# Performance work log

Hardware: AMD Instinct MI355X
Metric: run time of the kernel (lower is better)

## Reference

```python
import jax, jax.numpy as jnp
import numpy as np

NUM_EXPERTS = 4
TOPK = 1
TEMPERATURE = 1.0
NORM_TOPK_PROB = True
N_CLS = 1
N_REL = 4


def setup_inputs() -> dict:
    key = jax.random.key(0)
    ks = jax.random.split(key, 7)
    B, N_total, D, r, E = 64, 1029, 768, 64, NUM_EXPERTS
    x = jax.random.normal(ks[0], (B, N_total, D), dtype=jnp.float32)
    # parameters (torch Linear convention: weight [out, in])
    Wd = jax.random.normal(ks[1], (r, D), dtype=jnp.float32) * (1.0 / np.sqrt(D))
    Wg = jax.random.normal(ks[2], (E, r), dtype=jnp.float32) * (1.0 / np.sqrt(r))
    We = jax.random.normal(ks[3], (E, r, r), dtype=jnp.float32) * (1.0 / np.sqrt(r))
    be = jax.random.normal(ks[4], (E, r), dtype=jnp.float32) * 0.01
    Wu = jax.random.normal(ks[5], (D, r), dtype=jnp.float32) * (1.0 / np.sqrt(r))
    gamma = jnp.ones((D,), dtype=jnp.float32)  # LayerScale init_values=1.0
    return {"x": x, "Wd": Wd, "Wg": Wg, "We": We, "be": be, "Wu": Wu, "gamma": gamma}


def reference(x, Wd, Wg, We, be, Wu, gamma):
    # proj_down (bias=False) + exact GELU (nn.GELU default)
    h = jax.nn.gelu(jnp.einsum('bnd,rd->bnr', x, Wd), approximate=False)  # [B,Nt,r]
    cls_tok = h[:, :N_CLS, :]
    rel_tok = h[:, N_CLS:N_CLS + N_REL, :]
    t = h[:, N_CLS + N_REL:, :]                                           # [B,N,r]
    B, N, r = t.shape

    # gating: softmax scores, top-k selection
    logits = jnp.einsum('bnr,er->bne', t, Wg) / TEMPERATURE
    scores = jax.nn.softmax(logits, axis=-1)                              # [B,N,E]
    topk_w, topk_idx = jax.lax.top_k(scores, TOPK)                        # [B,N,K]
    if TOPK > 1 and NORM_TOPK_PROB:
        topk_w = topk_w / jnp.sum(topk_w, axis=-1, keepdims=True)

    # experts are tiny Linear(r,r): compute all experts densely, then gather.
    # Same math as per-expert gather/GEMM/scatter-combine in the source.
    expert_all = jnp.einsum('bnr,esr->bnes', t, We) + be                  # [B,N,E,r]
    idx_b = jnp.broadcast_to(topk_idx[..., None], (B, N, TOPK, r))
    sel = jnp.take_along_axis(expert_all, idx_b, axis=2)                  # [B,N,K,r]
    combine = jnp.sum(sel * topk_w[..., None], axis=2)                    # [B,N,r]

    full = jnp.concatenate([cls_tok, rel_tok, t + combine], axis=1)       # [B,Nt,r]
    # proj_up (bias=False) + LayerScale
    return jnp.einsum('bnr,dr->bnd', full, Wu) * gamma
```

## Files before the change

### kernel.cpp

```cpp
#include <hip/hip_runtime.h>
#include <math.h>


#define GELU(v) (0.5f*(v)*(1.0f + erff((v)*0.70710678118654752440f)))

typedef __attribute__((ext_vector_type(8))) short bf16x8;
typedef __attribute__((ext_vector_type(4))) float f32x4;

#define MFMA(a,b,c) __builtin_amdgcn_mfma_f32_16x16x32_bf16((a),(b),(c),0,0,0)

__device__ __forceinline__ unsigned pk_hi(float a, float b) {
  return (__float_as_uint(a) >> 16) | (__float_as_uint(b) & 0xFFFF0000u);
}
__device__ __forceinline__ float f_lo(float a) {
  return a - __uint_as_float(__float_as_uint(a) & 0xFFFF0000u);
}
union U8 { unsigned u[4]; bf16x8 v; uint4 q; };
__device__ __forceinline__ bf16x8 hi8(float4 f0, float4 f1) {
  U8 r; r.u[0]=pk_hi(f0.x,f0.y); r.u[1]=pk_hi(f0.z,f0.w);
        r.u[2]=pk_hi(f1.x,f1.y); r.u[3]=pk_hi(f1.z,f1.w); return r.v;
}
__device__ __forceinline__ bf16x8 lo8(float4 f0, float4 f1) {
  U8 r; r.u[0]=pk_hi(f_lo(f0.x),f_lo(f0.y)); r.u[1]=pk_hi(f_lo(f0.z),f_lo(f0.w));
        r.u[2]=pk_hi(f_lo(f1.x),f_lo(f1.y)); r.u[3]=pk_hi(f_lo(f1.z),f_lo(f1.w)); return r.v;
}

__device__ __forceinline__ void cp16(const char* g, char* d, int lane) {
#if __has_builtin(__builtin_amdgcn_global_load_lds)
  __builtin_amdgcn_global_load_lds(
      (const __attribute__((address_space(1))) unsigned int*)g,
      (__attribute__((address_space(3))) unsigned int*)d, 16, 0, 0);
#else
  *(uint4*)(d + lane*16) = *(const uint4*)g;
#endif
}

__global__ __launch_bounds__(256) void prep_pack(
    const float* __restrict__ Wd, const float* __restrict__ Wg,
    const float* __restrict__ We, const float* __restrict__ Wu,
    char* __restrict__ wp)
{
  int fid = blockIdx.x*4 + (threadIdx.x >> 6);
  if (fid >= 456) return;
  int l = threadIdx.x & 63, lg = l >> 4, lr = l & 15;
  float v[8];
  int part = 0;
  if (fid < 192) {
    int c = fid >> 3, s = fid & 7;
    int kt = c >> 1, kc = c & 1, nt = s >> 1; part = s & 1;
    const float* p = Wd + (size_t)(nt*16 + lr)*768 + kt*64 + kc*32 + lg*8;
    #pragma unroll
    for (int e = 0; e < 8; ++e) v[e] = p[e];
  } else if (fid < 264) {
    int f = fid - 192, ch = f >> 3, s = f & 7;
    if (ch == 0) {
      part = s & 1;
      int kc = (s >> 1) & 1;
      if (s < 4 && lr < 4) {
        const float* p = Wg + lr*64 + kc*32 + lg*8;
        #pragma unroll
        for (int e = 0; e < 8; ++e) v[e] = p[e];
      } else {
        #pragma unroll
        for (int e = 0; e < 8; ++e) v[e] = 0.f;
      }
    } else {
      int e_ = (ch - 1) >> 1, kc = (ch - 1) & 1, j = s >> 1; part = s & 1;
      const float* p = We + (size_t)(e_*64 + j*16 + lr)*64 + kc*32 + lg*8;
      #pragma unroll
      for (int e = 0; e < 8; ++e) v[e] = p[e];
    }
  } else {
    int f = fid - 264;
    int nt = f >> 2, kc = (f >> 1) & 1; part = f & 1;
    const float* p = Wu + (size_t)(nt*16 + lr)*64 + kc*32 + lg*8;
    #pragma unroll
    for (int e = 0; e < 8; ++e) v[e] = p[e];
  }
  U8 rr;
  if (part == 0) {
    rr.u[0]=pk_hi(v[0],v[1]); rr.u[1]=pk_hi(v[2],v[3]);
    rr.u[2]=pk_hi(v[4],v[5]); rr.u[3]=pk_hi(v[6],v[7]);
  } else {
    rr.u[0]=pk_hi(f_lo(v[0]),f_lo(v[1])); rr.u[1]=pk_hi(f_lo(v[2]),f_lo(v[3]));
    rr.u[2]=pk_hi(f_lo(v[4]),f_lo(v[5])); rr.u[3]=pk_hi(f_lo(v[6]),f_lo(v[7]));
  }
  *(uint4*)(wp + (size_t)fid*1024 + (size_t)l*16) = rr.q;
}

__global__ __launch_bounds__(256, 4) void fused(
    const float* __restrict__ x, const float* __restrict__ be,
    const float* __restrict__ gamma, const char* __restrict__ wp,
    float* __restrict__ out)
{
  __shared__ float sF[4][16][68];
  __shared__ char stage[2][8192];
  const int tid = threadIdx.x, bm = blockIdx.x;
  const int wv = tid >> 6, l = tid & 63, lg = l >> 4, lr = l & 15;
  const int tokbase = bm*64 + wv*16 + lg*4;

#define STAGE(chunk, buf) do { \
    const char* _g = wp + (size_t)(chunk)*8192 + (size_t)(wv*2)*1024 + (size_t)l*16; \
    char* _d = &stage[buf][wv*2048]; \
    cp16(_g, _d, l); \
    cp16(_g + 1024, _d + 1024, l); \
  } while (0)

  const float* xrow = x + (size_t)(bm*64 + wv*16 + lr)*768 + lg*8;
  f32x4 t4[4];
  #pragma unroll
  for (int nt = 0; nt < 4; ++nt)
    #pragma unroll
    for (int r = 0; r < 4; ++r) t4[nt][r] = 0.f;

  float4 xa = *(const float4*)xrow, xb = *(const float4*)(xrow + 4);
  STAGE(0, 0);
  __syncthreads();
  for (int c = 0; c < 24; ++c) {
    float4 xa2 = xa, xb2 = xb;
    if (c < 23) {
      STAGE(c + 1, (c + 1) & 1);
      const float* xp = xrow + (c + 1)*32;
      xa2 = *(const float4*)xp; xb2 = *(const float4*)(xp + 4);
    }
    bf16x8 ah = hi8(xa, xb), al = lo8(xa, xb);
    const char* bp = &stage[c & 1][l*16];
    #pragma unroll
    for (int nt = 0; nt < 4; ++nt) {
      bf16x8 bh = *(const bf16x8*)(bp + (size_t)(nt*2)*1024);
      bf16x8 bl = *(const bf16x8*)(bp + (size_t)(nt*2 + 1)*1024);
      t4[nt] = MFMA(ah, bh, t4[nt]);
      t4[nt] = MFMA(ah, bl, t4[nt]);
      t4[nt] = MFMA(al, bh, t4[nt]);
    }
    __syncthreads();
    xa = xa2; xb = xb2;
  }

  STAGE(24, 0);
  STAGE(25, 1);
  #pragma unroll
  for (int nt = 0; nt < 4; ++nt)
    #pragma unroll
    for (int r = 0; r < 4; ++r) {
      float g = GELU(t4[nt][r]);
      t4[nt][r] = g;
      sF[wv][lg*4 + r][nt*16 + lr] = g;
    }
  bf16x8 pah[2], pal[2];
  #pragma unroll
  for (int kc = 0; kc < 2; ++kc) {
    const float* ap = &sF[wv][lr][kc*32 + lg*8];
    float4 a0 = *(const float4*)ap, a1 = *(const float4*)(ap + 4);
    pah[kc] = hi8(a0, a1); pal[kc] = lo8(a0, a1);
  }
  __syncthreads();

  f32x4 lac;
  #pragma unroll
  for (int r = 0; r < 4; ++r) lac[r] = 0.f;
  {
    const char* bp = &stage[0][l*16];
    bf16x8 b0h = *(const bf16x8*)(bp);
    bf16x8 b0l = *(const bf16x8*)(bp + 1024);
    bf16x8 b1h = *(const bf16x8*)(bp + 2048);
    bf16x8 b1l = *(const bf16x8*)(bp + 3072);
    lac = MFMA(pah[0], b0h, lac); lac = MFMA(pah[0], b0l, lac); lac = MFMA(pal[0], b0h, lac);
    lac = MFMA(pah[1], b1h, lac); lac = MFMA(pah[1], b1l, lac); lac = MFMA(pal[1], b1h, lac);
  }
  float w_[4]; int ei_[4];
  #pragma unroll
  for (int r = 0; r < 4; ++r) {
    float lt = lac[r];
    int base = l & 48;
    float l0 = __shfl(lt, base + 0), l1 = __shfl(lt, base + 1);
    float l2 = __shfl(lt, base + 2), l3 = __shfl(lt, base + 3);
    int ei = 0; float lm = l0;
    if (l1 > lm) { lm = l1; ei = 1; }
    if (l2 > lm) { lm = l2; ei = 2; }
    if (l3 > lm) { lm = l3; ei = 3; }
    float s = expf(l0 - lm) + expf(l1 - lm) + expf(l2 - lm) + expf(l3 - lm);
    float w = 1.0f / s;
    int pos = (tokbase + r) % 1029;
    if (pos < 5) w = 0.0f;
    w_[r] = w; ei_[r] = ei;
  }
  __syncthreads();
  STAGE(26, 0);

  f32x4 de[4], sel[4];
  #pragma unroll
  for (int j = 0; j < 4; ++j)
    #pragma unroll
    for (int r = 0; r < 4; ++r) { de[j][r] = 0.f; sel[j][r] = 0.f; }

  #pragma unroll
  for (int s = 1; s <= 8; ++s) {
    const int e_ = (s - 1) >> 1, kc = (s - 1) & 1, cb = s & 1;
    const char* bp = &stage[cb][l*16];
    #pragma unroll
    for (int j = 0; j < 4; ++j) {
      bf16x8 bh = *(const bf16x8*)(bp + (size_t)(j*2)*1024);
      bf16x8 bl = *(const bf16x8*)(bp + (size_t)(j*2 + 1)*1024);
      de[j] = MFMA(pah[kc], bh, de[j]);
      de[j] = MFMA(pah[kc], bl, de[j]);
      de[j] = MFMA(pal[kc], bh, de[j]);
    }
    if (kc == 1) {
      #pragma unroll
      for (int j = 0; j < 4; ++j)
        #pragma unroll
        for (int r = 0; r < 4; ++r) {
          sel[j][r] = (ei_[r] == e_) ? de[j][r] : sel[j][r];
          de[j][r] = 0.f;
        }
    }
    __syncthreads();
    if (s <= 6) STAGE(26 + s, cb);
  }

  STAGE(33, 1);
  STAGE(34, 0);
  #pragma unroll
  for (int r = 0; r < 4; ++r)
    #pragma unroll
    for (int j = 0; j < 4; ++j) {
      int col = j*16 + lr;
      float full = t4[j][r] + w_[r] * (sel[j][r] + be[ei_[r]*64 + col]);
      sF[wv][lg*4 + r][col] = full;
    }
  bf16x8 a3h[2], a3l[2];
  #pragma unroll
  for (int kc = 0; kc < 2; ++kc) {
    const float* ap = &sF[wv][lr][kc*32 + lg*8];
    float4 a0 = *(const float4*)ap, a1 = *(const float4*)(ap + 4);
    a3h[kc] = hi8(a0, a1); a3l[kc] = lo8(a0, a1);
  }
  __syncthreads();

  for (int c = 0; c < 24; ++c) {
    const int cb = (c + 1) & 1;
    const char* bpc = &stage[cb][l*16];
    #pragma unroll
    for (int u = 0; u < 2; ++u) {
      const char* bp = bpc + u*4096;
      bf16x8 b0h = *(const bf16x8*)(bp);
      bf16x8 b0l = *(const bf16x8*)(bp + 1024);
      bf16x8 b1h = *(const bf16x8*)(bp + 2048);
      bf16x8 b1l = *(const bf16x8*)(bp + 3072);
      f32x4 o;
      #pragma unroll
      for (int r = 0; r < 4; ++r) o[r] = 0.f;
      o = MFMA(a3h[0], b0h, o); o = MFMA(a3h[0], b0l, o); o = MFMA(a3l[0], b0h, o);
      o = MFMA(a3h[1], b1h, o); o = MFMA(a3h[1], b1l, o); o = MFMA(a3l[1], b1h, o);
      const int col = (c*2 + u)*16 + lr;
      const float gv = gamma[col];
      #pragma unroll
      for (int r = 0; r < 4; ++r)
        out[(size_t)(tokbase + r)*768 + col] = o[r] * gv;
    }
    __syncthreads();
    if (c + 2 < 24) STAGE(35 + c, cb);
  }
#undef STAGE
}

extern "C" void kernel_launch(void* const* d_in, const int* in_sizes, int n_in,
                              void* d_out, int out_size, void* d_ws, size_t ws_size,
                              hipStream_t stream) {
  const float* x     = (const float*)d_in[0];
  const float* Wd    = (const float*)d_in[1];
  const float* Wg    = (const float*)d_in[2];
  const float* We    = (const float*)d_in[3];
  const float* be    = (const float*)d_in[4];
  const float* Wu    = (const float*)d_in[5];
  const float* gamma = (const float*)d_in[6];
  float* out = (float*)d_out;
  char* wp   = (char*)d_ws;

  prep_pack<<<114, 256, 0, stream>>>(Wd, Wg, We, Wu, wp);
  fused<<<1029, 256, 0, stream>>>(x, be, gamma, (const char*)wp, out);
}
```

Baseline: 428.7 us.

## Load packed weights directly into registers and drop LDS staging and barriers

Removes the double-buffered LDS stage and its global_load_lds copies. Each wave now reads the pre-packed bf16 weight fragments straight from global memory (L2-resident) into register double buffers, which eliminates almost all __syncthreads. It also adds a 4-deep register prefetch queue for x, preloads the expert biases to replace a gathered load, and lowers the occupancy hint to 3 waves because register pressure grows. The trade-off is redundant per-wave global/L2 traffic for the weights and lower occupancy.

```diff
diff --git a/kernel.cpp b/kernel.cpp
--- a/kernel.cpp
+++ b/kernel.cpp
@@ -23,16 +23,6 @@
 __device__ __forceinline__ bf16x8 lo8(float4 f0, float4 f1) {
   U8 r; r.u[0]=pk_hi(f_lo(f0.x),f_lo(f0.y)); r.u[1]=pk_hi(f_lo(f0.z),f_lo(f0.w));
         r.u[2]=pk_hi(f_lo(f1.x),f_lo(f1.y)); r.u[3]=pk_hi(f_lo(f1.z),f_lo(f1.w)); return r.v;
-}
-
-__device__ __forceinline__ void cp16(const char* g, char* d, int lane) {
-#if __has_builtin(__builtin_amdgcn_global_load_lds)
-  __builtin_amdgcn_global_load_lds(
-      (const __attribute__((address_space(1))) unsigned int*)g,
-      (__attribute__((address_space(3))) unsigned int*)d, 16, 0, 0);
-#else
-  *(uint4*)(d + lane*16) = *(const uint4*)g;
-#endif
 }
 
 __global__ __launch_bounds__(256) void prep_pack(
@@ -88,23 +78,16 @@
   *(uint4*)(wp + (size_t)fid*1024 + (size_t)l*16) = rr.q;
 }
 
-__global__ __launch_bounds__(256, 4) void fused(
+__global__ __launch_bounds__(256, 3) void fused(
     const float* __restrict__ x, const float* __restrict__ be,
     const float* __restrict__ gamma, const char* __restrict__ wp,
     float* __restrict__ out)
 {
   __shared__ float sF[4][16][68];
-  __shared__ char stage[2][8192];
   const int tid = threadIdx.x, bm = blockIdx.x;
   const int wv = tid >> 6, l = tid & 63, lg = l >> 4, lr = l & 15;
   const int tokbase = bm*64 + wv*16 + lg*4;
-
-#define STAGE(chunk, buf) do { \
-    const char* _g = wp + (size_t)(chunk)*8192 + (size_t)(wv*2)*1024 + (size_t)l*16; \
-    char* _d = &stage[buf][wv*2048]; \
-    cp16(_g, _d, l); \
-    cp16(_g + 1024, _d + 1024, l); \
-  } while (0)
+  const char* wpL = wp + (size_t)l*16;
 
   const float* xrow = x + (size_t)(bm*64 + wv*16 + lr)*768 + lg*8;
   f32x4 t4[4];
@@ -113,32 +96,66 @@
     #pragma unroll
     for (int r = 0; r < 4; ++r) t4[nt][r] = 0.f;
 
-  float4 xa = *(const float4*)xrow, xb = *(const float4*)(xrow + 4);
-  STAGE(0, 0);
-  __syncthreads();
-  for (int c = 0; c < 24; ++c) {
-    float4 xa2 = xa, xb2 = xb;
-    if (c < 23) {
-      STAGE(c + 1, (c + 1) & 1);
-      const float* xp = xrow + (c + 1)*32;
-      xa2 = *(const float4*)xp; xb2 = *(const float4*)(xp + 4);
-    }
-    bf16x8 ah = hi8(xa, xb), al = lo8(xa, xb);
-    const char* bp = &stage[c & 1][l*16];
-    #pragma unroll
-    for (int nt = 0; nt < 4; ++nt) {
-      bf16x8 bh = *(const bf16x8*)(bp + (size_t)(nt*2)*1024);
-      bf16x8 bl = *(const bf16x8*)(bp + (size_t)(nt*2 + 1)*1024);
-      t4[nt] = MFMA(ah, bh, t4[nt]);
-      t4[nt] = MFMA(ah, bl, t4[nt]);
-      t4[nt] = MFMA(al, bh, t4[nt]);
-    }
-    __syncthreads();
-    xa = xa2; xb = xb2;
-  }
-
-  STAGE(24, 0);
-  STAGE(25, 1);
+  float4 xqa[4], xqb[4];
+  #pragma unroll
+  for (int i = 0; i < 4; ++i) {
+    xqa[i] = *(const float4*)(xrow + i*32);
+    xqb[i] = *(const float4*)(xrow + i*32 + 4);
+  }
+  bf16x8 Bb[2][8];
+  #pragma unroll
+  for (int s = 0; s < 8; ++s)
+    Bb[0][s] = *(const bf16x8*)(wpL + (size_t)s*1024);
+
+#define P1_STEP(CBASE, I, DO_REFILL, DO_PF) do {                              \
+    const int c_ = (CBASE) + (I);                                             \
+    if (DO_PF) {                                                              \
+      _Pragma("unroll")                                                       \
+      for (int s = 0; s < 8; ++s)                                             \
+        Bb[((I)+1)&1][s] =                                                    \
+            *(const bf16x8*)(wpL + (size_t)((c_+1)*8 + s)*1024);              \
+    }                                                                         \
+    bf16x8 ah = hi8(xqa[(I)&3], xqb[(I)&3]);                                  \
+    bf16x8 al = lo8(xqa[(I)&3], xqb[(I)&3]);                                  \
+    if (DO_REFILL) {                                                          \
+      xqa[(I)&3] = *(const float4*)(xrow + (c_+4)*32);                        \
+      xqb[(I)&3] = *(const float4*)(xrow + (c_+4)*32 + 4);                    \
+    }                                                                         \
+    _Pragma("unroll")                                                         \
+    for (int nt = 0; nt < 4; ++nt) {                                          \
+      t4[nt] = MFMA(ah, Bb[(I)&1][nt*2],   t4[nt]);                           \
+      t4[nt] = MFMA(ah, Bb[(I)&1][nt*2+1], t4[nt]);                           \
+      t4[nt] = MFMA(al, Bb[(I)&1][nt*2],   t4[nt]);                           \
+    }                                                                         \
+  } while (0)
+
+  for (int cc = 0; cc < 20; cc += 4) {
+    P1_STEP(cc, 0, 1, 1);
+    P1_STEP(cc, 1, 1, 1);
+    P1_STEP(cc, 2, 1, 1);
+    P1_STEP(cc, 3, 1, 1);
+  }
+  P1_STEP(20, 0, 0, 1);
+  P1_STEP(20, 1, 0, 1);
+  P1_STEP(20, 2, 0, 1);
+  P1_STEP(20, 3, 0, 0);
+#undef P1_STEP
+
+  float beq[4][4];
+  #pragma unroll
+  for (int e = 0; e < 4; ++e)
+    #pragma unroll
+    for (int j = 0; j < 4; ++j)
+      beq[e][j] = be[e*64 + j*16 + lr];
+  bf16x8 g0h = *(const bf16x8*)(wpL + (size_t)192*1024);
+  bf16x8 g0l = *(const bf16x8*)(wpL + (size_t)193*1024);
+  bf16x8 g1h = *(const bf16x8*)(wpL + (size_t)194*1024);
+  bf16x8 g1l = *(const bf16x8*)(wpL + (size_t)195*1024);
+  bf16x8 Eb[2][8];
+  #pragma unroll
+  for (int s = 0; s < 8; ++s)
+    Eb[0][s] = *(const bf16x8*)(wpL + (size_t)(200 + s)*1024);
+
   #pragma unroll
   for (int nt = 0; nt < 4; ++nt)
     #pragma unroll
@@ -154,20 +171,13 @@
     float4 a0 = *(const float4*)ap, a1 = *(const float4*)(ap + 4);
     pah[kc] = hi8(a0, a1); pal[kc] = lo8(a0, a1);
   }
-  __syncthreads();
 
   f32x4 lac;
   #pragma unroll
   for (int r = 0; r < 4; ++r) lac[r] = 0.f;
-  {
-    const char* bp = &stage[0][l*16];
-    bf16x8 b0h = *(const bf16x8*)(bp);
-    bf16x8 b0l = *(const bf16x8*)(bp + 1024);
-    bf16x8 b1h = *(const bf16x8*)(bp + 2048);
-    bf16x8 b1l = *(const bf16x8*)(bp + 3072);
-    lac = MFMA(pah[0], b0h, lac); lac = MFMA(pah[0], b0l, lac); lac = MFMA(pal[0], b0h, lac);
-    lac = MFMA(pah[1], b1h, lac); lac = MFMA(pah[1], b1l, lac); lac = MFMA(pal[1], b1h, lac);
-  }
+  lac = MFMA(pah[0], g0h, lac); lac = MFMA(pah[0], g0l, lac); lac = MFMA(pal[0], g0h, lac);
+  lac = MFMA(pah[1], g1h, lac); lac = MFMA(pah[1], g1l, lac); lac = MFMA(pal[1], g1h, lac);
+
   float w_[4]; int ei_[4];
   #pragma unroll
   for (int r = 0; r < 4; ++r) {
@@ -185,8 +195,6 @@
     if (pos < 5) w = 0.0f;
     w_[r] = w; ei_[r] = ei;
   }
-  __syncthreads();
-  STAGE(26, 0);
 
   f32x4 de[4], sel[4];
   #pragma unroll
@@ -195,18 +203,21 @@
     for (int r = 0; r < 4; ++r) { de[j][r] = 0.f; sel[j][r] = 0.f; }
 
   #pragma unroll
-  for (int s = 1; s <= 8; ++s) {
-    const int e_ = (s - 1) >> 1, kc = (s - 1) & 1, cb = s & 1;
-    const char* bp = &stage[cb][l*16];
+  for (int st = 0; st < 8; ++st) {
+    if (st < 7) {
+      #pragma unroll
+      for (int s = 0; s < 8; ++s)
+        Eb[(st+1)&1][s] = *(const bf16x8*)(wpL + (size_t)(200 + (st+1)*8 + s)*1024);
+    }
+    const int kc = st & 1;
     #pragma unroll
     for (int j = 0; j < 4; ++j) {
-      bf16x8 bh = *(const bf16x8*)(bp + (size_t)(j*2)*1024);
-      bf16x8 bl = *(const bf16x8*)(bp + (size_t)(j*2 + 1)*1024);
-      de[j] = MFMA(pah[kc], bh, de[j]);
-      de[j] = MFMA(pah[kc], bl, de[j]);
-      de[j] = MFMA(pal[kc], bh, de[j]);
+      de[j] = MFMA(pah[kc], Eb[st&1][j*2],   de[j]);
+      de[j] = MFMA(pah[kc], Eb[st&1][j*2+1], de[j]);
+      de[j] = MFMA(pal[kc], Eb[st&1][j*2],   de[j]);
     }
     if (kc == 1) {
+      const int e_ = st >> 1;
       #pragma unroll
       for (int j = 0; j < 4; ++j)
         #pragma unroll
@@ -215,19 +226,19 @@
           de[j][r] = 0.f;
         }
     }
-    __syncthreads();
-    if (s <= 6) STAGE(26 + s, cb);
-  }
-
-  STAGE(33, 1);
-  STAGE(34, 0);
+  }
+
   #pragma unroll
   for (int r = 0; r < 4; ++r)
     #pragma unroll
     for (int j = 0; j < 4; ++j) {
-      int col = j*16 + lr;
-      float full = t4[j][r] + w_[r] * (sel[j][r] + be[ei_[r]*64 + col]);
-      sF[wv][lg*4 + r][col] = full;
+      float b0 = beq[0][j], b1 = beq[1][j], b2 = beq[2][j], b3 = beq[3][j];
+      float bsel = b0;
+      bsel = (ei_[r] == 1) ? b1 : bsel;
+      bsel = (ei_[r] == 2) ? b2 : bsel;
+      bsel = (ei_[r] == 3) ? b3 : bsel;
+      float full = t4[j][r] + w_[r] * (sel[j][r] + bsel);
+      sF[wv][lg*4 + r][j*16 + lr] = full;
     }
   bf16x8 a3h[2], a3l[2];
   #pragma unroll
@@ -236,33 +247,43 @@
     float4 a0 = *(const float4*)ap, a1 = *(const float4*)(ap + 4);
     a3h[kc] = hi8(a0, a1); a3l[kc] = lo8(a0, a1);
   }
-  __syncthreads();
-
-  for (int c = 0; c < 24; ++c) {
-    const int cb = (c + 1) & 1;
-    const char* bpc = &stage[cb][l*16];
-    #pragma unroll
-    for (int u = 0; u < 2; ++u) {
-      const char* bp = bpc + u*4096;
-      bf16x8 b0h = *(const bf16x8*)(bp);
-      bf16x8 b0l = *(const bf16x8*)(bp + 1024);
-      bf16x8 b1h = *(const bf16x8*)(bp + 2048);
-      bf16x8 b1l = *(const bf16x8*)(bp + 3072);
-      f32x4 o;
-      #pragma unroll
-      for (int r = 0; r < 4; ++r) o[r] = 0.f;
-      o = MFMA(a3h[0], b0h, o); o = MFMA(a3h[0], b0l, o); o = MFMA(a3l[0], b0h, o);
-      o = MFMA(a3h[1], b1h, o); o = MFMA(a3h[1], b1l, o); o = MFMA(a3l[1], b1h, o);
-      const int col = (c*2 + u)*16 + lr;
-      const float gv = gamma[col];
-      #pragma unroll
-      for (int r = 0; r < 4; ++r)
-        out[(size_t)(tokbase + r)*768 + col] = o[r] * gv;
-    }
-    __syncthreads();
-    if (c + 2 < 24) STAGE(35 + c, cb);
-  }
-#undef STAGE
+
+  bf16x8 Wb[2][4];
+  float gq[2];
+  #pragma unroll
+  for (int f = 0; f < 4; ++f)
+    Wb[0][f] = *(const bf16x8*)(wpL + (size_t)(264 + f)*1024);
+  gq[0] = gamma[lr];
+
+#define P3_STEP(NT, CUR, NXT, DO_PF) do {                                     \
+    if (DO_PF) {                                                              \
+      _Pragma("unroll")                                                       \
+      for (int f = 0; f < 4; ++f)                                             \
+        Wb[NXT][f] =                                                          \
+            *(const bf16x8*)(wpL + (size_t)(264 + ((NT)+1)*4 + f)*1024);      \
+      gq[NXT] = gamma[((NT)+1)*16 + lr];                                      \
+    }                                                                         \
+    f32x4 o;                                                                  \
+    _Pragma("unroll") for (int r = 0; r < 4; ++r) o[r] = 0.f;                 \
+    o = MFMA(a3h[0], Wb[CUR][0], o);                                          \
+    o = MFMA(a3h[0], Wb[CUR][1], o);                                          \
+    o = MFMA(a3l[0], Wb[CUR][0], o);                                          \
+    o = MFMA(a3h[1], Wb[CUR][2], o);                                          \
+    o = MFMA(a3h[1], Wb[CUR][3], o);                                          \
+    o = MFMA(a3l[1], Wb[CUR][2], o);                                          \
+    const int col_ = (NT)*16 + lr;                                            \
+    const float gv_ = gq[CUR];                                                \
+    _Pragma("unroll") for (int r = 0; r < 4; ++r)                             \
+      out[(size_t)(tokbase + r)*768 + col_] = o[r]*gv_;                       \
+  } while (0)
+
+  for (int q = 0; q < 23; ++q) {
+    P3_STEP(2*q,     0, 1, 1);
+    P3_STEP(2*q + 1, 1, 0, 1);
+  }
+  P3_STEP(46, 0, 1, 1);
+  P3_STEP(47, 1, 0, 0);
+#undef P3_STEP
 }
 
 extern "C" void kernel_launch(void* const* d_in, const int* in_sizes, int n_in,
```

Result: no change. 436.0 us (+1.7%).

## Split token tile across wave pairs and read packed weights directly from global

Applied to the files above, without the earlier changes.

Drops the LDS double-buffered weight staging and the per-chunk block barriers; each wave now loads packed bf16 weight fragments straight from global memory (L2/L1 cached). Blocks now cover 32 tokens, with wave pairs splitting the down-projection and up-projection output columns, doubling the grid and raising the occupancy hint to 6. This cuts register and LDS use and synchronisation cost, in exchange for redundant global weight reads per wave and the expert GEMM being computed twice per token group.

```diff
diff --git a/kernel.cpp b/kernel.cpp
--- a/kernel.cpp
+++ b/kernel.cpp
@@ -23,16 +23,6 @@
 __device__ __forceinline__ bf16x8 lo8(float4 f0, float4 f1) {
   U8 r; r.u[0]=pk_hi(f_lo(f0.x),f_lo(f0.y)); r.u[1]=pk_hi(f_lo(f0.z),f_lo(f0.w));
         r.u[2]=pk_hi(f_lo(f1.x),f_lo(f1.y)); r.u[3]=pk_hi(f_lo(f1.z),f_lo(f1.w)); return r.v;
-}
-
-__device__ __forceinline__ void cp16(const char* g, char* d, int lane) {
-#if __has_builtin(__builtin_amdgcn_global_load_lds)
-  __builtin_amdgcn_global_load_lds(
-      (const __attribute__((address_space(1))) unsigned int*)g,
-      (__attribute__((address_space(3))) unsigned int*)d, 16, 0, 0);
-#else
-  *(uint4*)(d + lane*16) = *(const uint4*)g;
-#endif
 }
 
 __global__ __launch_bounds__(256) void prep_pack(
@@ -88,85 +78,67 @@
   *(uint4*)(wp + (size_t)fid*1024 + (size_t)l*16) = rr.q;
 }
 
-__global__ __launch_bounds__(256, 4) void fused(
+__global__ __launch_bounds__(256, 6) void fused(
     const float* __restrict__ x, const float* __restrict__ be,
     const float* __restrict__ gamma, const char* __restrict__ wp,
     float* __restrict__ out)
 {
-  __shared__ float sF[4][16][68];
-  __shared__ char stage[2][8192];
+  __shared__ float sT[2][16][68];
+  __shared__ float sFull[2][16][68];
   const int tid = threadIdx.x, bm = blockIdx.x;
   const int wv = tid >> 6, l = tid & 63, lg = l >> 4, lr = l & 15;
-  const int tokbase = bm*64 + wv*16 + lg*4;
-
-#define STAGE(chunk, buf) do { \
-    const char* _g = wp + (size_t)(chunk)*8192 + (size_t)(wv*2)*1024 + (size_t)l*16; \
-    char* _d = &stage[buf][wv*2048]; \
-    cp16(_g, _d, l); \
-    cp16(_g + 1024, _d + 1024, l); \
-  } while (0)
-
-  const float* xrow = x + (size_t)(bm*64 + wv*16 + lr)*768 + lg*8;
-  f32x4 t4[4];
-  #pragma unroll
-  for (int nt = 0; nt < 4; ++nt)
-    #pragma unroll
-    for (int r = 0; r < 4; ++r) t4[nt][r] = 0.f;
-
-  float4 xa = *(const float4*)xrow, xb = *(const float4*)(xrow + 4);
-  STAGE(0, 0);
+  const int g = wv >> 1, u = wv & 1;
+  const int tokg = bm*32 + g*16;
+  const char* wpL = wp + (size_t)l*16;
+
+  const float* xrow = x + (size_t)(tokg + lr)*768 + lg*8;
+  f32x4 t4[2];
+  #pragma unroll
+  for (int j = 0; j < 2; ++j)
+    #pragma unroll
+    for (int r = 0; r < 4; ++r) t4[j][r] = 0.f;
+
+  #pragma unroll 2
+  for (int c = 0; c < 24; ++c) {
+    float4 f0 = *(const float4*)(xrow + c*32);
+    float4 f1 = *(const float4*)(xrow + c*32 + 4);
+    bf16x8 ah = hi8(f0, f1), al = lo8(f0, f1);
+    const char* bp = wpL + (size_t)(c*8 + u*4)*1024;
+    #pragma unroll
+    for (int j = 0; j < 2; ++j) {
+      bf16x8 bh = *(const bf16x8*)(bp + (size_t)(j*2)*1024);
+      bf16x8 bl = *(const bf16x8*)(bp + (size_t)(j*2 + 1)*1024);
+      t4[j] = MFMA(ah, bh, t4[j]);
+      t4[j] = MFMA(ah, bl, t4[j]);
+      t4[j] = MFMA(al, bh, t4[j]);
+    }
+  }
+  #pragma unroll
+  for (int j = 0; j < 2; ++j)
+    #pragma unroll
+    for (int r = 0; r < 4; ++r)
+      sT[g][lg*4 + r][(u*2 + j)*16 + lr] = GELU(t4[j][r]);
+
   __syncthreads();
-  for (int c = 0; c < 24; ++c) {
-    float4 xa2 = xa, xb2 = xb;
-    if (c < 23) {
-      STAGE(c + 1, (c + 1) & 1);
-      const float* xp = xrow + (c + 1)*32;
-      xa2 = *(const float4*)xp; xb2 = *(const float4*)(xp + 4);
-    }
-    bf16x8 ah = hi8(xa, xb), al = lo8(xa, xb);
-    const char* bp = &stage[c & 1][l*16];
-    #pragma unroll
-    for (int nt = 0; nt < 4; ++nt) {
-      bf16x8 bh = *(const bf16x8*)(bp + (size_t)(nt*2)*1024);
-      bf16x8 bl = *(const bf16x8*)(bp + (size_t)(nt*2 + 1)*1024);
-      t4[nt] = MFMA(ah, bh, t4[nt]);
-      t4[nt] = MFMA(ah, bl, t4[nt]);
-      t4[nt] = MFMA(al, bh, t4[nt]);
-    }
-    __syncthreads();
-    xa = xa2; xb = xb2;
-  }
-
-  STAGE(24, 0);
-  STAGE(25, 1);
-  #pragma unroll
-  for (int nt = 0; nt < 4; ++nt)
-    #pragma unroll
-    for (int r = 0; r < 4; ++r) {
-      float g = GELU(t4[nt][r]);
-      t4[nt][r] = g;
-      sF[wv][lg*4 + r][nt*16 + lr] = g;
-    }
+
   bf16x8 pah[2], pal[2];
   #pragma unroll
   for (int kc = 0; kc < 2; ++kc) {
-    const float* ap = &sF[wv][lr][kc*32 + lg*8];
+    const float* ap = &sT[g][lr][kc*32 + lg*8];
     float4 a0 = *(const float4*)ap, a1 = *(const float4*)(ap + 4);
     pah[kc] = hi8(a0, a1); pal[kc] = lo8(a0, a1);
   }
-  __syncthreads();
 
   f32x4 lac;
   #pragma unroll
   for (int r = 0; r < 4; ++r) lac[r] = 0.f;
   {
-    const char* bp = &stage[0][l*16];
-    bf16x8 b0h = *(const bf16x8*)(bp);
-    bf16x8 b0l = *(const bf16x8*)(bp + 1024);
-    bf16x8 b1h = *(const bf16x8*)(bp + 2048);
-    bf16x8 b1l = *(const bf16x8*)(bp + 3072);
-    lac = MFMA(pah[0], b0h, lac); lac = MFMA(pah[0], b0l, lac); lac = MFMA(pal[0], b0h, lac);
-    lac = MFMA(pah[1], b1h, lac); lac = MFMA(pah[1], b1l, lac); lac = MFMA(pal[1], b1h, lac);
+    bf16x8 g0h = *(const bf16x8*)(wpL + (size_t)192*1024);
+    bf16x8 g0l = *(const bf16x8*)(wpL + (size_t)193*1024);
+    bf16x8 g1h = *(const bf16x8*)(wpL + (size_t)194*1024);
+    bf16x8 g1l = *(const bf16x8*)(wpL + (size_t)195*1024);
+    lac = MFMA(pah[0], g0h, lac); lac = MFMA(pah[0], g0l, lac); lac = MFMA(pal[0], g0h, lac);
+    lac = MFMA(pah[1], g1h, lac); lac = MFMA(pah[1], g1l, lac); lac = MFMA(pal[1], g1h, lac);
   }
   float w_[4]; int ei_[4];
   #pragma unroll
@@ -181,88 +153,84 @@
     if (l3 > lm) { lm = l3; ei = 3; }
     float s = expf(l0 - lm) + expf(l1 - lm) + expf(l2 - lm) + expf(l3 - lm);
     float w = 1.0f / s;
-    int pos = (tokbase + r) % 1029;
+    int pos = (tokg + lg*4 + r) % 1029;
     if (pos < 5) w = 0.0f;
     w_[r] = w; ei_[r] = ei;
   }
-  __syncthreads();
-  STAGE(26, 0);
-
-  f32x4 de[4], sel[4];
+
+  f32x4 sel[4];
   #pragma unroll
   for (int j = 0; j < 4; ++j)
     #pragma unroll
-    for (int r = 0; r < 4; ++r) { de[j][r] = 0.f; sel[j][r] = 0.f; }
-
-  #pragma unroll
-  for (int s = 1; s <= 8; ++s) {
-    const int e_ = (s - 1) >> 1, kc = (s - 1) & 1, cb = s & 1;
-    const char* bp = &stage[cb][l*16];
-    #pragma unroll
-    for (int j = 0; j < 4; ++j) {
-      bf16x8 bh = *(const bf16x8*)(bp + (size_t)(j*2)*1024);
-      bf16x8 bl = *(const bf16x8*)(bp + (size_t)(j*2 + 1)*1024);
-      de[j] = MFMA(pah[kc], bh, de[j]);
-      de[j] = MFMA(pah[kc], bl, de[j]);
-      de[j] = MFMA(pal[kc], bh, de[j]);
-    }
-    if (kc == 1) {
-      #pragma unroll
-      for (int j = 0; j < 4; ++j)
-        #pragma unroll
-        for (int r = 0; r < 4; ++r) {
-          sel[j][r] = (ei_[r] == e_) ? de[j][r] : sel[j][r];
-          de[j][r] = 0.f;
+    for (int r = 0; r < 4; ++r) sel[j][r] = 0.f;
+
+  #pragma unroll
+  for (int e = 0; e < 4; ++e) {
+    #pragma unroll
+    for (int jh = 0; jh < 2; ++jh) {
+      f32x4 de[2];
+      #pragma unroll
+      for (int jj = 0; jj < 2; ++jj)
+        #pragma unroll
+        for (int r = 0; r < 4; ++r) de[jj][r] = 0.f;
+      #pragma unroll
+      for (int kc = 0; kc < 2; ++kc) {
+        const char* bp = wpL + (size_t)(200 + (e*2 + kc)*8)*1024;
+        #pragma unroll
+        for (int jj = 0; jj < 2; ++jj) {
+          const int j = jh*2 + jj;
+          bf16x8 bh = *(const bf16x8*)(bp + (size_t)(j*2)*1024);
+          bf16x8 bl = *(const bf16x8*)(bp + (size_t)(j*2 + 1)*1024);
+          de[jj] = MFMA(pah[kc], bh, de[jj]);
+          de[jj] = MFMA(pah[kc], bl, de[jj]);
+          de[jj] = MFMA(pal[kc], bh, de[jj]);
         }
-    }
-    __syncthreads();
-    if (s <= 6) STAGE(26 + s, cb);
-  }
-
-  STAGE(33, 1);
-  STAGE(34, 0);
+      }
+      #pragma unroll
+      for (int jj = 0; jj < 2; ++jj)
+        #pragma unroll
+        for (int r = 0; r < 4; ++r)
+          sel[jh*2 + jj][r] = (ei_[r] == e) ? de[jj][r] : sel[jh*2 + jj][r];
+    }
+  }
+
   #pragma unroll
   for (int r = 0; r < 4; ++r)
     #pragma unroll
     for (int j = 0; j < 4; ++j) {
       int col = j*16 + lr;
-      float full = t4[j][r] + w_[r] * (sel[j][r] + be[ei_[r]*64 + col]);
-      sF[wv][lg*4 + r][col] = full;
-    }
+      float tv = sT[g][lg*4 + r][col];
+      float bev = be[ei_[r]*64 + col];
+      sFull[g][lg*4 + r][col] = tv + w_[r] * (sel[j][r] + bev);
+    }
+
   bf16x8 a3h[2], a3l[2];
   #pragma unroll
   for (int kc = 0; kc < 2; ++kc) {
-    const float* ap = &sF[wv][lr][kc*32 + lg*8];
+    const float* ap = &sFull[g][lr][kc*32 + lg*8];
     float4 a0 = *(const float4*)ap, a1 = *(const float4*)(ap + 4);
     a3h[kc] = hi8(a0, a1); a3l[kc] = lo8(a0, a1);
   }
-  __syncthreads();
-
-  for (int c = 0; c < 24; ++c) {
-    const int cb = (c + 1) & 1;
-    const char* bpc = &stage[cb][l*16];
-    #pragma unroll
-    for (int u = 0; u < 2; ++u) {
-      const char* bp = bpc + u*4096;
-      bf16x8 b0h = *(const bf16x8*)(bp);
-      bf16x8 b0l = *(const bf16x8*)(bp + 1024);
-      bf16x8 b1h = *(const bf16x8*)(bp + 2048);
-      bf16x8 b1l = *(const bf16x8*)(bp + 3072);
-      f32x4 o;
-      #pragma unroll
-      for (int r = 0; r < 4; ++r) o[r] = 0.f;
-      o = MFMA(a3h[0], b0h, o); o = MFMA(a3h[0], b0l, o); o = MFMA(a3l[0], b0h, o);
-      o = MFMA(a3h[1], b1h, o); o = MFMA(a3h[1], b1l, o); o = MFMA(a3l[1], b1h, o);
-      const int col = (c*2 + u)*16 + lr;
-      const float gv = gamma[col];
-      #pragma unroll
-      for (int r = 0; r < 4; ++r)
-        out[(size_t)(tokbase + r)*768 + col] = o[r] * gv;
-    }
-    __syncthreads();
-    if (c + 2 < 24) STAGE(35 + c, cb);
-  }
-#undef STAGE
+
+  #pragma unroll 2
+  for (int q = 0; q < 24; ++q) {
+    const int nt = u*24 + q;
+    const char* bp = wpL + (size_t)(264 + nt*4)*1024;
+    bf16x8 b0h = *(const bf16x8*)(bp);
+    bf16x8 b0l = *(const bf16x8*)(bp + 1024);
+    bf16x8 b1h = *(const bf16x8*)(bp + 2048);
+    bf16x8 b1l = *(const bf16x8*)(bp + 3072);
+    f32x4 o;
+    #pragma unroll
+    for (int r = 0; r < 4; ++r) o[r] = 0.f;
+    o = MFMA(a3h[0], b0h, o); o = MFMA(a3h[0], b0l, o); o = MFMA(a3l[0], b0h, o);
+    o = MFMA(a3h[1], b1h, o); o = MFMA(a3h[1], b1l, o); o = MFMA(a3l[1], b1h, o);
+    const int col = nt*16 + lr;
+    const float gv = gamma[col];
+    #pragma unroll
+    for (int r = 0; r < 4; ++r)
+      out[(size_t)(tokg + lg*4 + r)*768 + col] = o[r] * gv;
+  }
 }
 
 extern "C" void kernel_launch(void* const* d_in, const int* in_sizes, int n_in,
@@ -279,5 +247,5 @@
   char* wp   = (char*)d_ws;
 
   prep_pack<<<114, 256, 0, stream>>>(Wd, Wg, We, Wu, wp);
-  fused<<<1029, 256, 0, stream>>>(x, be, gamma, (const char*)wp, out);
-}
+  fused<<<2058, 256, 0, stream>>>(x, be, gamma, (const char*)wp, out);
+}
```

Result: slower. 450.6 us (+5.1%).
